# Kernel optimization log

Hardware: AMD Instinct MI355X
Metric: run time of the kernel (lower is better)

The kernel has to match this reference:

```python
import jax, jax.numpy as jnp
import numpy as np

EPS = 1e-5
HEADS, DK, DV = 8, 32, 64
SCALE = DK ** -0.5

def _bn(x, gamma, beta, mean, var):
    # eval-mode BatchNorm1d over channel dim of [b, c, n]
    inv = gamma / jnp.sqrt(var + EPS)
    return (x - mean[None, :, None]) * inv[None, :, None] + beta[None, :, None]

def setup_inputs() -> dict:
    key = jax.random.key(0)
    ks = jax.random.split(key, 24)
    dim, n, dim_out = 256, 1024, 256
    idk, idv = DK * HEADS, DV * HEADS
    def bn_params(k, c):
        k1, k2, k3, k4 = jax.random.split(k, 4)
        return (jax.random.normal(k1, (c,)) * 0.1 + 1.0,   # gamma
                jax.random.normal(k2, (c,)) * 0.1,          # beta
                jax.random.normal(k3, (c,)) * 0.1,          # running mean
                jax.random.uniform(k4, (c,)) * 0.5 + 0.5)   # running var > 0
    q_g, q_b, q_m, q_v = bn_params(ks[1], idk)
    k_g, k_b, k_m, k_v = bn_params(ks[2], idk)
    v_g, v_b, v_m, v_v = bn_params(ks[3], idv)
    o_g, o_b, o_m, o_v = bn_params(ks[4], dim_out)
    return {
        'x': jax.random.normal(ks[0], (8, dim, n), dtype=jnp.float32),
        'Wq': jax.random.normal(ks[5], (idk, dim)) * (dim ** -0.5),
        'Wk': jax.random.normal(ks[6], (idk, dim)) * (dim ** -0.5),
        'Wv': jax.random.normal(ks[7], (idv, dim)) * (dim ** -0.5),
        'Wo': jax.random.normal(ks[8], (dim_out, idv)) * (idv ** -0.5),
        'bo': jax.random.normal(ks[9], (dim_out,)) * 0.02,
        'pos_emb': jax.random.normal(ks[10], (n, HEADS)) * 0.02,
        'q_gamma': q_g, 'q_beta': q_b, 'q_mean': q_m, 'q_var': q_v,
        'k_gamma': k_g, 'k_beta': k_b, 'k_mean': k_m, 'k_var': k_v,
        'v_gamma': v_g, 'v_beta': v_b, 'v_mean': v_m, 'v_var': v_v,
        'o_gamma': o_g, 'o_beta': o_b, 'o_mean': o_m, 'o_var': o_v,
    }

def reference(x, Wq, Wk, Wv, Wo, bo, pos_emb,
              q_gamma, q_beta, q_mean, q_var,
              k_gamma, k_beta, k_mean, k_var,
              v_gamma, v_beta, v_mean, v_var,
              o_gamma, o_beta, o_mean, o_var):
    b, _, n = x.shape
    # 1x1 conv == channel matmul, then BN
    q = _bn(jnp.einsum('bcn,oc->bon', x, Wq), q_gamma, q_beta, q_mean, q_var)
    k = _bn(jnp.einsum('bcn,oc->bon', x, Wk), k_gamma, k_beta, k_mean, k_var)
    v = _bn(jnp.einsum('bcn,oc->bon', x, Wv), v_gamma, v_beta, v_mean, v_var)
    # b (h d) n -> b h n d
    q = q.reshape(b, HEADS, DK, n).transpose(0, 1, 3, 2)
    k = k.reshape(b, HEADS, DK, n).transpose(0, 1, 3, 2)
    v = v.reshape(b, HEADS, DV, n).transpose(0, 1, 3, 2)
    dots = jnp.einsum('bhid,bhjd->bhij', q, k) * SCALE
    # relative-position bias: emb[|i-j|] -> [n, n, h] -> [1, h, n, n]
    rel = jnp.abs(jnp.arange(n)[:, None] - jnp.arange(n)[None, :])
    bias = pos_emb[rel].transpose(2, 0, 1)[None]
    dots = dots + bias / SCALE
    attn = jax.nn.softmax(dots, axis=-1)
    out = jnp.einsum('bhij,bhjd->bhid', attn, v)
    # b h n d -> b (h d) n
    out = out.transpose(0, 1, 3, 2).reshape(b, HEADS * DV, n)
    out = jax.nn.gelu(out, approximate=False)
    out = jnp.einsum('bcn,oc->bon', out, Wo) + bo[None, :, None]
    return _bn(out, o_gamma, o_beta, o_mean, o_var)
```

## Files before the change

kernel.cpp:

```cpp
#include <hip/hip_runtime.h>
#include <hip/hip_bf16.h>

#define HEADS 8
#define DK 32
#define DV 64
#define DIM 256
#define NCTX 1024
#define NB 8
#define IDK 256
#define IDV 512
#define SCALE 0.17677669529663687f
#define INV_SCALE 5.656854249492381f
#define BN_EPS 1e-5f
#define THR 8.0f

typedef __bf16 bf16x8 __attribute__((ext_vector_type(8)));
typedef __bf16 bf16x4 __attribute__((ext_vector_type(4)));
typedef float f32x4 __attribute__((ext_vector_type(4)));
typedef float f32x16 __attribute__((ext_vector_type(16)));

static __device__ __forceinline__ unsigned short bfbits(float v) {
  __bf16 b = (__bf16)v;
  return __builtin_bit_cast(unsigned short, b);
}

__global__ __launch_bounds__(256) void k_prep_trans(
    const float* __restrict__ x,
    const float* __restrict__ Wq, const float* __restrict__ Wk,
    const float* __restrict__ Wv, const float* __restrict__ Wo,
    const float* __restrict__ bo, const float* __restrict__ pe,
    const float* __restrict__ qg, const float* __restrict__ qb,
    const float* __restrict__ qm, const float* __restrict__ qv,
    const float* __restrict__ kg, const float* __restrict__ kb,
    const float* __restrict__ km, const float* __restrict__ kv,
    const float* __restrict__ vg, const float* __restrict__ vb,
    const float* __restrict__ vm, const float* __restrict__ vv,
    const float* __restrict__ og, const float* __restrict__ ob,
    const float* __restrict__ om, const float* __restrict__ ov,
    __bf16* __restrict__ xT, __bf16* __restrict__ WB, float* __restrict__ BB,
    uint2* __restrict__ Tq4g) {
  int bid = blockIdx.x;
  if (bid < 1605) {
    int idx = bid * 256 + threadIdx.x;
    if (idx < 65536) {
      int o = idx >> 8;
      WB[idx] = (__bf16)(Wq[idx] * (qg[o] * rsqrtf(qv[o] + BN_EPS) * SCALE));
    } else if (idx < 131072) {
      int i = idx - 65536, o = i >> 8;
      WB[idx] = (__bf16)(Wk[i] * (kg[o] * rsqrtf(kv[o] + BN_EPS)));
    } else if (idx < 262144) {
      int i = idx - 131072, o = i >> 8;
      WB[idx] = (__bf16)(Wv[i] * (vg[o] * rsqrtf(vv[o] + BN_EPS)));
    } else if (idx < 393216) {
      int i = idx - 262144, o = i >> 9;
      WB[idx] = (__bf16)(Wo[i] * (og[o] * rsqrtf(ov[o] + BN_EPS)));
    } else if (idx < 394496) {
      int i = idx - 393216;
      if (i < 256) {
        float sc = qg[i] * rsqrtf(qv[i] + BN_EPS);
        BB[i] = (qb[i] - qm[i] * sc) * SCALE;
      } else if (i < 512) {
        int o = i - 256;
        float sc = kg[o] * rsqrtf(kv[o] + BN_EPS);
        BB[i] = kb[o] - km[o] * sc;
      } else if (i < 1024) {
        int o = i - 512;
        float sc = vg[o] * rsqrtf(vv[o] + BN_EPS);
        BB[i] = vb[o] - vm[o] * sc;
      } else {
        int o = i - 1024;
        float sc = og[o] * rsqrtf(ov[o] + BN_EPS);
        BB[i] = (bo[o] - om[o]) * sc + ob[o];
      }
    } else {
      int i = idx - 394496;
      int h = i >> 11, t = i & 2047;
      unsigned short us[4];
#pragma unroll
      for (int rr = 0; rr < 4; ++rr) {
        int d = t - rr - 1023; d = d < 0 ? -d : d; d = d > 1023 ? 1023 : d;
        us[rr] = bfbits(pe[(size_t)d * HEADS + h] * INV_SCALE);
      }
      uint2 e;
      e.x = (unsigned)us[0] | ((unsigned)us[1] << 16);
      e.y = (unsigned)us[2] | ((unsigned)us[3] << 16);
      Tq4g[((size_t)h << 11) + t] = e;
    }
  } else {
    __shared__ float t[64][65];
    int tb = bid - 1605;
    int b = tb >> 6, c0 = ((tb >> 4) & 3) * 64, n0 = (tb & 15) * 64;
    int col = threadIdx.x & 63, rb = threadIdx.x >> 6;
    const float* xp = x + ((size_t)b * DIM + c0) * NCTX + n0;
#pragma unroll
    for (int r = 0; r < 16; ++r) {
      int row = rb + 4 * r;
      t[row][col] = xp[(size_t)row * NCTX + col];
    }
    __syncthreads();
    __bf16* op = xT + ((size_t)b * NCTX + n0) * DIM + c0;
#pragma unroll
    for (int r = 0; r < 16; ++r) {
      int i = rb + 4 * r;
      op[(size_t)i * DIM + col] = (__bf16)t[col][i];
    }
  }
}

__global__ __launch_bounds__(256, 2) void k_gemm(
    const __bf16* __restrict__ Xsrc, const __bf16* __restrict__ Wsrc,
    const float* __restrict__ Bias, __bf16* __restrict__ Qws,
    __bf16* __restrict__ Kws, __bf16* __restrict__ Vws,
    float* __restrict__ Oout, int lda, int ksteps, int mode_base) {
  int bx = blockIdx.x, by = blockIdx.y;
  int mode = (mode_base == 3) ? 3 : (by < 2 ? 0 : (by < 4 ? 1 : 2));
  int tid = threadIdx.x, wave = tid >> 6, lane = tid & 63;
  int wm = wave >> 1, wn = wave & 1;
  int l16 = lane & 15, g = (lane >> 4) & 3, g4 = g * 4;
  int R0 = bx * 128;

  __shared__ __align__(16) char XTl[16384];
  __shared__ __align__(16) char WTl[16384];

  int sr = tid >> 1, sh = tid & 1;
  const __bf16* xg = Xsrc + (size_t)(R0 + sr) * lda + sh * 32;
  const __bf16* wg = Wsrc + (size_t)(by * 128 + sr) * lda + sh * 32;
  int wbase = sr * 128;
  int gsw[4];
#pragma unroll
  for (int q = 0; q < 4; ++q) gsw[q] = ((sh * 4 + q) ^ (sr & 7)) * 16;

  bf16x8 sx[4], sw[4];
#pragma unroll
  for (int q = 0; q < 4; ++q) {
    sx[q] = *reinterpret_cast<const bf16x8*>(xg + q * 8);
    sw[q] = *reinterpret_cast<const bf16x8*>(wg + q * 8);
  }

  f32x4 acc[4][4] = {};
  const char* Abase = (mode <= 1) ? WTl : XTl;
  const char* Bbase = (mode <= 1) ? XTl : WTl;

  for (int st = 0; st < ksteps; ++st) {
    __syncthreads();
#pragma unroll
    for (int q = 0; q < 4; ++q) {
      *reinterpret_cast<bf16x8*>(XTl + wbase + gsw[q]) = sx[q];
      *reinterpret_cast<bf16x8*>(WTl + wbase + gsw[q]) = sw[q];
    }
    __syncthreads();
    if (st + 1 < ksteps) {
      const __bf16* xn = xg + (st + 1) * 64;
      const __bf16* wn_ = wg + (st + 1) * 64;
#pragma unroll
      for (int q = 0; q < 4; ++q) {
        sx[q] = *reinterpret_cast<const bf16x8*>(xn + q * 8);
        sw[q] = *reinterpret_cast<const bf16x8*>(wn_ + q * 8);
      }
    }
#pragma unroll
    for (int kc = 0; kc < 2; ++kc) {
      bf16x8 af[4], bf[4];
#pragma unroll
      for (int t = 0; t < 4; ++t) {
        int ra = wm * 64 + t * 16 + l16;
        af[t] = *reinterpret_cast<const bf16x8*>(
            Abase + ra * 128 + (((kc * 4 + g) ^ (ra & 7)) * 16));
        int rb = wn * 64 + t * 16 + l16;
        bf[t] = *reinterpret_cast<const bf16x8*>(
            Bbase + rb * 128 + (((kc * 4 + g) ^ (rb & 7)) * 16));
      }
#pragma unroll
      for (int mt = 0; mt < 4; ++mt)
#pragma unroll
        for (int nt = 0; nt < 4; ++nt)
          acc[mt][nt] = __builtin_amdgcn_mfma_f32_16x16x32_bf16(
              af[mt], bf[nt], acc[mt][nt], 0, 0, 0);
    }
  }

  if (mode <= 1) {
    __bf16* OWS = (mode == 0) ? Qws : Kws;
    const float* bb = Bias + (mode == 0 ? 0 : 256);
    int oq0 = by * 128 - (mode == 1 ? 256 : 0) + wm * 64;
#pragma unroll
    for (int mt = 0; mt < 4; ++mt) {
      int oq = oq0 + mt * 16 + g4;
      float4 b4 = *reinterpret_cast<const float4*>(&bb[oq]);
      int h = oq >> 5, d0 = oq & 31;
#pragma unroll
      for (int nt = 0; nt < 4; ++nt) {
        int i = R0 + wn * 64 + nt * 16 + l16;
        int b = i >> 10, n = i & 1023;
        bf16x4 pk;
        pk[0] = (__bf16)(acc[mt][nt][0] + b4.x);
        pk[1] = (__bf16)(acc[mt][nt][1] + b4.y);
        pk[2] = (__bf16)(acc[mt][nt][2] + b4.z);
        pk[3] = (__bf16)(acc[mt][nt][3] + b4.w);
        *reinterpret_cast<bf16x4*>(
            &OWS[(((size_t)b * HEADS + h) * NCTX + n) * DK + d0]) = pk;
      }
    }
  } else if (mode == 2) {
#pragma unroll
    for (int nt = 0; nt < 4; ++nt) {
      int vo = (by - 4) * 128 + wn * 64 + nt * 16 + l16;
      float bia = Bias[512 + vo];
#pragma unroll
      for (int mt = 0; mt < 4; ++mt) {
        int i0 = R0 + wm * 64 + mt * 16 + g4;
        int b = i0 >> 10, n = i0 & 1023;
        bf16x4 pk;
#pragma unroll
        for (int rr = 0; rr < 4; ++rr) pk[rr] = (__bf16)(acc[mt][nt][rr] + bia);
        *reinterpret_cast<bf16x4*>(&Vws[((size_t)b * IDV + vo) * NCTX + n]) = pk;
      }
    }
  } else {
#pragma unroll
    for (int nt = 0; nt < 4; ++nt) {
      int o = by * 128 + wn * 64 + nt * 16 + l16;
      float bia = Bias[o];
#pragma unroll
      for (int mt = 0; mt < 4; ++mt) {
        int i0 = R0 + wm * 64 + mt * 16 + g4;
        int b = i0 >> 10, n = i0 & 1023;
        float4 st;
        st.x = acc[mt][nt][0] + bia;
        st.y = acc[mt][nt][1] + bia;
        st.z = acc[mt][nt][2] + bia;
        st.w = acc[mt][nt][3] + bia;
        *reinterpret_cast<float4*>(&Oout[((size_t)b * DIM + o) * NCTX + n]) = st;
      }
    }
  }
}

__global__ __launch_bounds__(256, 2) void k_attn(
    const __bf16* __restrict__ Qws, const __bf16* __restrict__ Kws,
    const __bf16* __restrict__ Vws, const uint2* __restrict__ Tq4g,
    __bf16* __restrict__ G) {
  int flat = blockIdx.x;
  int swz = (flat & 7) * 64 + (flat >> 3);
  int iblk = swz & 7, bh = swz >> 3;
  int b = bh >> 3, h = bh & 7;
  int tid = threadIdx.x, wave = tid >> 6, lane = tid & 63;
  int l31 = lane & 31, hi = lane >> 5;

  __shared__ __align__(16) __bf16 Klds[64][40];
  __shared__ __align__(16) __bf16 Vlds[64 * 64];
  __shared__ __align__(16) uint2 TqL[1152];

  int i0b = iblk * 128;
  {
    const uint4* tg4 = reinterpret_cast<const uint4*>(Tq4g + ((size_t)h << 11) + i0b);
    uint4* tl4 = reinterpret_cast<uint4*>(TqL);
    for (int c = tid; c < 576; c += 256) tl4[c] = tg4[c];
  }

  int i0w = i0b + wave * 32;
  int irow = i0w + l31;
  const __bf16* qbase = Qws + (size_t)bh * NCTX * DK;
  const __bf16* kbase = Kws + (size_t)bh * NCTX * DK;
  const __bf16* vbase = Vws + ((size_t)b * IDV + h * DV) * NCTX;
  bf16x8 qf0 = *reinterpret_cast<const bf16x8*>(qbase + (size_t)irow * DK + 8 * hi);
  bf16x8 qf1 = *reinterpret_cast<const bf16x8*>(qbase + (size_t)irow * DK + 16 + 8 * hi);

  int r_ = tid >> 2, sk = tid & 3;
  const __bf16* kgp = kbase + (size_t)r_ * DK + 8 * sk;
  const __bf16* vgp = vbase + (size_t)r_ * NCTX + 8 * sk;
  __bf16* kw = &Klds[r_][8 * sk];
  __bf16* vw0 = Vlds + r_ * 64 + 8 * (sk ^ (r_ & 7));
  __bf16* vw1 = Vlds + r_ * 64 + 8 * ((sk + 4) ^ (r_ & 7));

  bf16x8 rk = *reinterpret_cast<const bf16x8*>(kgp);
  bf16x8 rv0 = *reinterpret_cast<const bf16x8*>(vgp);
  bf16x8 rv1 = *reinterpret_cast<const bf16x8*>(vgp + 32);

  f32x16 acc0 = {}, acc1 = {};
  float m = -1e30f, s = 0.0f;
  int kxb = wave * 32 + l31 + 1023 - 4 * hi;
  const bf16x4* Tqp = reinterpret_cast<const bf16x4*>(TqL);

  for (int it = 0; it < 16; ++it) {
    int j0 = it * 64;
    __syncthreads();
    *reinterpret_cast<bf16x8*>(kw) = rk;
    *reinterpret_cast<bf16x8*>(vw0) = rv0;
    *reinterpret_cast<bf16x8*>(vw1) = rv1;
    __syncthreads();
    int jn = (j0 + 64) & (NCTX - 1);
    rk = *reinterpret_cast<const bf16x8*>(kgp + (size_t)jn * DK);
    rv0 = *reinterpret_cast<const bf16x8*>(vgp + jn);
    rv1 = *reinterpret_cast<const bf16x8*>(vgp + jn + 32);

    float sv[32];
#pragma unroll
    for (int jg = 0; jg < 2; ++jg) {
      bf16x8 kf0 = *reinterpret_cast<const bf16x8*>(&Klds[32 * jg + l31][8 * hi]);
      bf16x8 kf1 = *reinterpret_cast<const bf16x8*>(&Klds[32 * jg + l31][16 + 8 * hi]);
      f32x16 S = {};
      S = __builtin_amdgcn_mfma_f32_32x32x16_bf16(kf0, qf0, S, 0, 0, 0);
      S = __builtin_amdgcn_mfma_f32_32x32x16_bf16(kf1, qf1, S, 0, 0, 0);
      int kb_ = kxb - j0 - 32 * jg;
#pragma unroll
      for (int q = 0; q < 4; ++q) {
        bf16x4 q4 = Tqp[kb_ - 8 * q];
#pragma unroll
        for (int rr = 0; rr < 4; ++rr)
          sv[jg * 16 + q * 4 + rr] = S[q * 4 + rr] + (float)q4[rr];
      }
    }
    float pmax = sv[0];
#pragma unroll
    for (int k = 1; k < 32; ++k) pmax = fmaxf(pmax, sv[k]);
    if (__any(pmax > m + THR)) {
      float mx = fmaxf(pmax, __shfl_xor(pmax, 32));
      float mnew = fmaxf(m, mx);
      float corr = __expf(m - mnew);
      s *= corr; m = mnew;
#pragma unroll
      for (int r = 0; r < 16; ++r) {
        float cv = __shfl(corr, (r & 3) + 8 * (r >> 2) + 4 * hi);
        acc0[r] *= cv; acc1[r] *= cv;
      }
    }
#pragma unroll
    for (int k = 0; k < 32; ++k) sv[k] = __expf(sv[k] - m);
    float ps = 0.0f;
#pragma unroll
    for (int k = 0; k < 32; ++k) ps += sv[k];
    s += ps;
#pragma unroll
    for (int jg = 0; jg < 2; ++jg) {
#pragma unroll
      for (int u = 0; u < 2; ++u) {
        int base = jg * 16 + 8 * u;
        unsigned we0, we1, wo0, wo1;
        asm("v_cvt_pk_bf16_f32 %0, %1, %2" : "=v"(we0) : "v"(sv[base + 0]), "v"(sv[base + 1]));
        asm("v_cvt_pk_bf16_f32 %0, %1, %2" : "=v"(we1) : "v"(sv[base + 2]), "v"(sv[base + 3]));
        asm("v_cvt_pk_bf16_f32 %0, %1, %2" : "=v"(wo0) : "v"(sv[base + 4]), "v"(sv[base + 5]));
        asm("v_cvt_pk_bf16_f32 %0, %1, %2" : "=v"(wo1) : "v"(sv[base + 6]), "v"(sv[base + 7]));
        asm volatile("v_permlane32_swap_b32 %0, %1" : "+v"(we0), "+v"(wo0));
        asm volatile("v_permlane32_swap_b32 %0, %1" : "+v"(we1), "+v"(wo1));
        uint4 pw = {we0, we1, wo0, wo1};
        bf16x8 pfrag = *reinterpret_cast<bf16x8*>(&pw);
        int c = jg * 2 + u;
        int sl = 2 * c + hi;
        bf16x8 vf0 = *reinterpret_cast<const bf16x8*>(Vlds + l31 * 64 + 8 * (sl ^ (l31 & 7)));
        bf16x8 vf1 = *reinterpret_cast<const bf16x8*>(Vlds + (32 + l31) * 64 + 8 * (sl ^ (l31 & 7)));
        acc0 = __builtin_amdgcn_mfma_f32_32x32x16_bf16(pfrag, vf0, acc0, 0, 0, 0);
        acc1 = __builtin_amdgcn_mfma_f32_32x32x16_bf16(pfrag, vf1, acc1, 0, 0, 0);
      }
    }
  }
  float srow = s + __shfl_xor(s, 32);
  float inv = 1.0f / srow;
  __bf16* gbase = G + (size_t)b * NCTX * IDV + h * DV + l31;
#pragma unroll
  for (int r = 0; r < 16; ++r) {
    int il = (r & 3) + 8 * (r >> 2) + 4 * hi;
    float iv = __shfl(inv, il);
    float v0 = acc0[r] * iv, v1 = acc1[r] * iv;
    float g0 = 0.5f * v0 * (1.0f + erff(v0 * 0.70710678118654752f));
    float g1 = 0.5f * v1 * (1.0f + erff(v1 * 0.70710678118654752f));
    gbase[(size_t)(i0w + il) * IDV] = (__bf16)g0;
    gbase[(size_t)(i0w + il) * IDV + 32] = (__bf16)g1;
  }
}

extern "C" void kernel_launch(void* const* d_in, const int* in_sizes, int n_in,
                              void* d_out, int out_size, void* d_ws, size_t ws_size,
                              hipStream_t stream) {
  const float* x  = (const float*)d_in[0];
  const float* Wq = (const float*)d_in[1];
  const float* Wk = (const float*)d_in[2];
  const float* Wv = (const float*)d_in[3];
  const float* Wo = (const float*)d_in[4];
  const float* bo = (const float*)d_in[5];
  const float* pe = (const float*)d_in[6];
  const float* qg = (const float*)d_in[7];
  const float* qb = (const float*)d_in[8];
  const float* qm = (const float*)d_in[9];
  const float* qv = (const float*)d_in[10];
  const float* kg = (const float*)d_in[11];
  const float* kb = (const float*)d_in[12];
  const float* km = (const float*)d_in[13];
  const float* kv = (const float*)d_in[14];
  const float* vg = (const float*)d_in[15];
  const float* vb = (const float*)d_in[16];
  const float* vm = (const float*)d_in[17];
  const float* vv = (const float*)d_in[18];
  const float* og = (const float*)d_in[19];
  const float* ob = (const float*)d_in[20];
  const float* om = (const float*)d_in[21];
  const float* ov = (const float*)d_in[22];

  char* ws = (char*)d_ws;
  __bf16* xT = (__bf16*)(ws);
  __bf16* Q  = (__bf16*)(ws + (4ull << 20));
  __bf16* K  = (__bf16*)(ws + (8ull << 20));
  __bf16* V  = (__bf16*)(ws + (12ull << 20));
  __bf16* G  = (__bf16*)(ws + (20ull << 20));
  __bf16* WB = (__bf16*)(ws + (28ull << 20));
  float*  BB = (float*)(ws + (28ull << 20) + (768ull << 10));
  uint2*  Tq = (uint2*)(ws + (29ull << 20));
  float* out = (float*)d_out;

  k_prep_trans<<<dim3(2117), 256, 0, stream>>>(
      x, Wq, Wk, Wv, Wo, bo, pe, qg, qb, qm, qv, kg, kb, km, kv,
      vg, vb, vm, vv, og, ob, om, ov, xT, WB, BB, Tq);
  k_gemm<<<dim3(64, 8), 256, 0, stream>>>(xT, WB, BB, Q, K, V, nullptr,
                                          DIM, 4, 0);
  k_attn<<<dim3(512), 256, 0, stream>>>(Q, K, V, Tq, G);
  k_gemm<<<dim3(64, 2), 256, 0, stream>>>(G, WB + 262144, BB + 1024,
                                          nullptr, nullptr, nullptr, out,
                                          IDV, 8, 3);
}
```

Before: 63.57 us.

## Use exp2 softmax, smaller attention blocks, split output GEMM, MFMA priority hints

Measured after the change: 60.64 us. 4.6% less time.

```diff
diff --git a/kernel.cpp b/kernel.cpp
--- a/kernel.cpp
+++ b/kernel.cpp
@@ -11,8 +11,9 @@
 #define IDV 512
 #define SCALE 0.17677669529663687f
 #define INV_SCALE 5.656854249492381f
+#define LOG2E 1.4426950408889634f
 #define BN_EPS 1e-5f
-#define THR 8.0f
+#define THR 11.5416f
 
 typedef __bf16 bf16x8 __attribute__((ext_vector_type(8)));
 typedef __bf16 bf16x4 __attribute__((ext_vector_type(4)));
@@ -44,7 +45,7 @@
     int idx = bid * 256 + threadIdx.x;
     if (idx < 65536) {
       int o = idx >> 8;
-      WB[idx] = (__bf16)(Wq[idx] * (qg[o] * rsqrtf(qv[o] + BN_EPS) * SCALE));
+      WB[idx] = (__bf16)(Wq[idx] * (qg[o] * rsqrtf(qv[o] + BN_EPS) * SCALE * LOG2E));
     } else if (idx < 131072) {
       int i = idx - 65536, o = i >> 8;
       WB[idx] = (__bf16)(Wk[i] * (kg[o] * rsqrtf(kv[o] + BN_EPS)));
@@ -58,7 +59,7 @@
       int i = idx - 393216;
       if (i < 256) {
         float sc = qg[i] * rsqrtf(qv[i] + BN_EPS);
-        BB[i] = (qb[i] - qm[i] * sc) * SCALE;
+        BB[i] = (qb[i] - qm[i] * sc) * SCALE * LOG2E;
       } else if (i < 512) {
         int o = i - 256;
         float sc = kg[o] * rsqrtf(kv[o] + BN_EPS);
@@ -79,7 +80,7 @@
 #pragma unroll
       for (int rr = 0; rr < 4; ++rr) {
         int d = t - rr - 1023; d = d < 0 ? -d : d; d = d > 1023 ? 1023 : d;
-        us[rr] = bfbits(pe[(size_t)d * HEADS + h] * INV_SCALE);
+        us[rr] = bfbits(pe[(size_t)d * HEADS + h] * INV_SCALE * LOG2E);
       }
       uint2 e;
       e.x = (unsigned)us[0] | ((unsigned)us[1] << 16);
@@ -107,13 +108,12 @@
   }
 }
 
-__global__ __launch_bounds__(256, 2) void k_gemm(
+__global__ __launch_bounds__(256, 2) void k_gemm_qkv(
     const __bf16* __restrict__ Xsrc, const __bf16* __restrict__ Wsrc,
     const float* __restrict__ Bias, __bf16* __restrict__ Qws,
-    __bf16* __restrict__ Kws, __bf16* __restrict__ Vws,
-    float* __restrict__ Oout, int lda, int ksteps, int mode_base) {
+    __bf16* __restrict__ Kws, __bf16* __restrict__ Vws) {
   int bx = blockIdx.x, by = blockIdx.y;
-  int mode = (mode_base == 3) ? 3 : (by < 2 ? 0 : (by < 4 ? 1 : 2));
+  int mode = by < 2 ? 0 : (by < 4 ? 1 : 2);
   int tid = threadIdx.x, wave = tid >> 6, lane = tid & 63;
   int wm = wave >> 1, wn = wave & 1;
   int l16 = lane & 15, g = (lane >> 4) & 3, g4 = g * 4;
@@ -123,8 +123,8 @@
   __shared__ __align__(16) char WTl[16384];
 
   int sr = tid >> 1, sh = tid & 1;
-  const __bf16* xg = Xsrc + (size_t)(R0 + sr) * lda + sh * 32;
-  const __bf16* wg = Wsrc + (size_t)(by * 128 + sr) * lda + sh * 32;
+  const __bf16* xg = Xsrc + (size_t)(R0 + sr) * DIM + sh * 32;
+  const __bf16* wg = Wsrc + (size_t)(by * 128 + sr) * DIM + sh * 32;
   int wbase = sr * 128;
   int gsw[4];
 #pragma unroll
@@ -141,7 +141,7 @@
   const char* Abase = (mode <= 1) ? WTl : XTl;
   const char* Bbase = (mode <= 1) ? XTl : WTl;
 
-  for (int st = 0; st < ksteps; ++st) {
+  for (int st = 0; st < 4; ++st) {
     __syncthreads();
 #pragma unroll
     for (int q = 0; q < 4; ++q) {
@@ -149,7 +149,7 @@
       *reinterpret_cast<bf16x8*>(WTl + wbase + gsw[q]) = sw[q];
     }
     __syncthreads();
-    if (st + 1 < ksteps) {
+    if (st + 1 < 4) {
       const __bf16* xn = xg + (st + 1) * 64;
       const __bf16* wn_ = wg + (st + 1) * 64;
 #pragma unroll
@@ -170,12 +170,14 @@
         bf[t] = *reinterpret_cast<const bf16x8*>(
             Bbase + rb * 128 + (((kc * 4 + g) ^ (rb & 7)) * 16));
       }
+      __builtin_amdgcn_s_setprio(1);
 #pragma unroll
       for (int mt = 0; mt < 4; ++mt)
 #pragma unroll
         for (int nt = 0; nt < 4; ++nt)
           acc[mt][nt] = __builtin_amdgcn_mfma_f32_16x16x32_bf16(
               af[mt], bf[nt], acc[mt][nt], 0, 0, 0);
+      __builtin_amdgcn_s_setprio(0);
     }
   }
 
@@ -201,7 +203,7 @@
             &OWS[(((size_t)b * HEADS + h) * NCTX + n) * DK + d0]) = pk;
       }
     }
-  } else if (mode == 2) {
+  } else {
 #pragma unroll
     for (int nt = 0; nt < 4; ++nt) {
       int vo = (by - 4) * 128 + wn * 64 + nt * 16 + l16;
@@ -216,46 +218,121 @@
         *reinterpret_cast<bf16x4*>(&Vws[((size_t)b * IDV + vo) * NCTX + n]) = pk;
       }
     }
-  } else {
-#pragma unroll
-    for (int nt = 0; nt < 4; ++nt) {
-      int o = by * 128 + wn * 64 + nt * 16 + l16;
-      float bia = Bias[o];
-#pragma unroll
-      for (int mt = 0; mt < 4; ++mt) {
-        int i0 = R0 + wm * 64 + mt * 16 + g4;
-        int b = i0 >> 10, n = i0 & 1023;
-        float4 st;
-        st.x = acc[mt][nt][0] + bia;
-        st.y = acc[mt][nt][1] + bia;
-        st.z = acc[mt][nt][2] + bia;
-        st.w = acc[mt][nt][3] + bia;
-        *reinterpret_cast<float4*>(&Oout[((size_t)b * DIM + o) * NCTX + n]) = st;
-      }
-    }
   }
 }
 
-__global__ __launch_bounds__(256, 2) void k_attn(
+__global__ __launch_bounds__(256, 2) void k_gemm_out(
+    const __bf16* __restrict__ G, const __bf16* __restrict__ WoB,
+    const float* __restrict__ bo2, float* __restrict__ out) {
+  int bx = blockIdx.x, by = blockIdx.y;
+  int tid = threadIdx.x, wave = tid >> 6, lane = tid & 63;
+  int wm = wave >> 1, wn = wave & 1;
+  int l16 = lane & 15, g = (lane >> 4) & 3, g4 = g * 4;
+  int R0 = bx * 128;
+
+  __shared__ __align__(16) char XTl[16384];
+  __shared__ __align__(16) char WTl[8192];
+
+  int sr = tid >> 1, sh = tid & 1;
+  const __bf16* xg = G + (size_t)(R0 + sr) * IDV + sh * 32;
+  int xbase = sr * 128;
+  int gsw[4];
+#pragma unroll
+  for (int q = 0; q < 4; ++q) gsw[q] = ((sh * 4 + q) ^ (sr & 7)) * 16;
+
+  int wsr = tid >> 2, wq = tid & 3;
+  const __bf16* wg = WoB + (size_t)(by * 64 + wsr) * IDV + wq * 16;
+  int wbase = wsr * 128;
+  int gswW[2];
+#pragma unroll
+  for (int q = 0; q < 2; ++q) gswW[q] = ((wq * 2 + q) ^ (wsr & 7)) * 16;
+
+  bf16x8 sx[4], sw[2];
+#pragma unroll
+  for (int q = 0; q < 4; ++q) sx[q] = *reinterpret_cast<const bf16x8*>(xg + q * 8);
+#pragma unroll
+  for (int q = 0; q < 2; ++q) sw[q] = *reinterpret_cast<const bf16x8*>(wg + q * 8);
+
+  f32x4 acc[4][2] = {};
+
+  for (int st = 0; st < 8; ++st) {
+    __syncthreads();
+#pragma unroll
+    for (int q = 0; q < 4; ++q) *reinterpret_cast<bf16x8*>(XTl + xbase + gsw[q]) = sx[q];
+#pragma unroll
+    for (int q = 0; q < 2; ++q) *reinterpret_cast<bf16x8*>(WTl + wbase + gswW[q]) = sw[q];
+    __syncthreads();
+    if (st + 1 < 8) {
+      const __bf16* xn = xg + (st + 1) * 64;
+      const __bf16* wn_ = wg + (st + 1) * 64;
+#pragma unroll
+      for (int q = 0; q < 4; ++q) sx[q] = *reinterpret_cast<const bf16x8*>(xn + q * 8);
+#pragma unroll
+      for (int q = 0; q < 2; ++q) sw[q] = *reinterpret_cast<const bf16x8*>(wn_ + q * 8);
+    }
+#pragma unroll
+    for (int kc = 0; kc < 2; ++kc) {
+      bf16x8 af[4], bf[2];
+#pragma unroll
+      for (int t = 0; t < 4; ++t) {
+        int ra = wm * 64 + t * 16 + l16;
+        af[t] = *reinterpret_cast<const bf16x8*>(
+            XTl + ra * 128 + (((kc * 4 + g) ^ (ra & 7)) * 16));
+      }
+#pragma unroll
+      for (int t = 0; t < 2; ++t) {
+        int rb = wn * 32 + t * 16 + l16;
+        bf[t] = *reinterpret_cast<const bf16x8*>(
+            WTl + rb * 128 + (((kc * 4 + g) ^ (rb & 7)) * 16));
+      }
+      __builtin_amdgcn_s_setprio(1);
+#pragma unroll
+      for (int mt = 0; mt < 4; ++mt)
+#pragma unroll
+        for (int nt = 0; nt < 2; ++nt)
+          acc[mt][nt] = __builtin_amdgcn_mfma_f32_16x16x32_bf16(
+              af[mt], bf[nt], acc[mt][nt], 0, 0, 0);
+      __builtin_amdgcn_s_setprio(0);
+    }
+  }
+#pragma unroll
+  for (int nt = 0; nt < 2; ++nt) {
+    int o = by * 64 + wn * 32 + nt * 16 + l16;
+    float bia = bo2[o];
+#pragma unroll
+    for (int mt = 0; mt < 4; ++mt) {
+      int i0 = R0 + wm * 64 + mt * 16 + g4;
+      int b = i0 >> 10, n = i0 & 1023;
+      float4 st;
+      st.x = acc[mt][nt][0] + bia;
+      st.y = acc[mt][nt][1] + bia;
+      st.z = acc[mt][nt][2] + bia;
+      st.w = acc[mt][nt][3] + bia;
+      *reinterpret_cast<float4*>(&out[((size_t)b * DIM + o) * NCTX + n]) = st;
+    }
+  }
+}
+
+__global__ __launch_bounds__(128, 3) void k_attn(
     const __bf16* __restrict__ Qws, const __bf16* __restrict__ Kws,
     const __bf16* __restrict__ Vws, const uint2* __restrict__ Tq4g,
     __bf16* __restrict__ G) {
   int flat = blockIdx.x;
-  int swz = (flat & 7) * 64 + (flat >> 3);
-  int iblk = swz & 7, bh = swz >> 3;
+  int swz = (flat & 7) * 128 + (flat >> 3);
+  int iblk = swz & 15, bh = swz >> 4;
   int b = bh >> 3, h = bh & 7;
   int tid = threadIdx.x, wave = tid >> 6, lane = tid & 63;
   int l31 = lane & 31, hi = lane >> 5;
 
   __shared__ __align__(16) __bf16 Klds[64][40];
   __shared__ __align__(16) __bf16 Vlds[64 * 64];
-  __shared__ __align__(16) uint2 TqL[1152];
-
-  int i0b = iblk * 128;
+  __shared__ __align__(16) uint2 TqL[1088];
+
+  int i0b = iblk * 64;
   {
     const uint4* tg4 = reinterpret_cast<const uint4*>(Tq4g + ((size_t)h << 11) + i0b);
     uint4* tl4 = reinterpret_cast<uint4*>(TqL);
-    for (int c = tid; c < 576; c += 256) tl4[c] = tg4[c];
+    for (int c = tid; c < 544; c += 128) tl4[c] = tg4[c];
   }
 
   int i0w = i0b + wave * 32;
@@ -266,16 +343,22 @@
   bf16x8 qf0 = *reinterpret_cast<const bf16x8*>(qbase + (size_t)irow * DK + 8 * hi);
   bf16x8 qf1 = *reinterpret_cast<const bf16x8*>(qbase + (size_t)irow * DK + 16 + 8 * hi);
 
-  int r_ = tid >> 2, sk = tid & 3;
-  const __bf16* kgp = kbase + (size_t)r_ * DK + 8 * sk;
-  const __bf16* vgp = vbase + (size_t)r_ * NCTX + 8 * sk;
-  __bf16* kw = &Klds[r_][8 * sk];
-  __bf16* vw0 = Vlds + r_ * 64 + 8 * (sk ^ (r_ & 7));
-  __bf16* vw1 = Vlds + r_ * 64 + 8 * ((sk + 4) ^ (r_ & 7));
-
-  bf16x8 rk = *reinterpret_cast<const bf16x8*>(kgp);
+  int r_ = tid >> 1, s2 = (tid & 1) * 2;
+  const __bf16* kgp = kbase + (size_t)r_ * DK + 8 * s2;
+  const __bf16* vgp = vbase + (size_t)r_ * NCTX + 8 * s2;
+  __bf16* kw0 = &Klds[r_][8 * s2];
+  __bf16* kw1 = &Klds[r_][8 * (s2 + 1)];
+  __bf16* vw0 = Vlds + r_ * 64 + 8 * ((s2) ^ (r_ & 7));
+  __bf16* vw1 = Vlds + r_ * 64 + 8 * ((s2 + 1) ^ (r_ & 7));
+  __bf16* vw2 = Vlds + r_ * 64 + 8 * ((s2 + 4) ^ (r_ & 7));
+  __bf16* vw3 = Vlds + r_ * 64 + 8 * ((s2 + 5) ^ (r_ & 7));
+
+  bf16x8 rk0 = *reinterpret_cast<const bf16x8*>(kgp);
+  bf16x8 rk1 = *reinterpret_cast<const bf16x8*>(kgp + 8);
   bf16x8 rv0 = *reinterpret_cast<const bf16x8*>(vgp);
-  bf16x8 rv1 = *reinterpret_cast<const bf16x8*>(vgp + 32);
+  bf16x8 rv1 = *reinterpret_cast<const bf16x8*>(vgp + 8);
+  bf16x8 rv2 = *reinterpret_cast<const bf16x8*>(vgp + 32);
+  bf16x8 rv3 = *reinterpret_cast<const bf16x8*>(vgp + 40);
 
   f32x16 acc0 = {}, acc1 = {};
   float m = -1e30f, s = 0.0f;
@@ -285,14 +368,20 @@
   for (int it = 0; it < 16; ++it) {
     int j0 = it * 64;
     __syncthreads();
-    *reinterpret_cast<bf16x8*>(kw) = rk;
+    *reinterpret_cast<bf16x8*>(kw0) = rk0;
+    *reinterpret_cast<bf16x8*>(kw1) = rk1;
     *reinterpret_cast<bf16x8*>(vw0) = rv0;
     *reinterpret_cast<bf16x8*>(vw1) = rv1;
+    *reinterpret_cast<bf16x8*>(vw2) = rv2;
+    *reinterpret_cast<bf16x8*>(vw3) = rv3;
     __syncthreads();
     int jn = (j0 + 64) & (NCTX - 1);
-    rk = *reinterpret_cast<const bf16x8*>(kgp + (size_t)jn * DK);
+    rk0 = *reinterpret_cast<const bf16x8*>(kgp + (size_t)jn * DK);
+    rk1 = *reinterpret_cast<const bf16x8*>(kgp + (size_t)jn * DK + 8);
     rv0 = *reinterpret_cast<const bf16x8*>(vgp + jn);
-    rv1 = *reinterpret_cast<const bf16x8*>(vgp + jn + 32);
+    rv1 = *reinterpret_cast<const bf16x8*>(vgp + jn + 8);
+    rv2 = *reinterpret_cast<const bf16x8*>(vgp + jn + 32);
+    rv3 = *reinterpret_cast<const bf16x8*>(vgp + jn + 40);
 
     float sv[32];
 #pragma unroll
@@ -300,8 +389,10 @@
       bf16x8 kf0 = *reinterpret_cast<const bf16x8*>(&Klds[32 * jg + l31][8 * hi]);
       bf16x8 kf1 = *reinterpret_cast<const bf16x8*>(&Klds[32 * jg + l31][16 + 8 * hi]);
       f32x16 S = {};
+      __builtin_amdgcn_s_setprio(1);
       S = __builtin_amdgcn_mfma_f32_32x32x16_bf16(kf0, qf0, S, 0, 0, 0);
       S = __builtin_amdgcn_mfma_f32_32x32x16_bf16(kf1, qf1, S, 0, 0, 0);
+      __builtin_amdgcn_s_setprio(0);
       int kb_ = kxb - j0 - 32 * jg;
 #pragma unroll
       for (int q = 0; q < 4; ++q) {
@@ -317,7 +408,7 @@
     if (__any(pmax > m + THR)) {
       float mx = fmaxf(pmax, __shfl_xor(pmax, 32));
       float mnew = fmaxf(m, mx);
-      float corr = __expf(m - mnew);
+      float corr = __builtin_amdgcn_exp2f(m - mnew);
       s *= corr; m = mnew;
 #pragma unroll
       for (int r = 0; r < 16; ++r) {
@@ -326,7 +417,7 @@
       }
     }
 #pragma unroll
-    for (int k = 0; k < 32; ++k) sv[k] = __expf(sv[k] - m);
+    for (int k = 0; k < 32; ++k) sv[k] = __builtin_amdgcn_exp2f(sv[k] - m);
     float ps = 0.0f;
 #pragma unroll
     for (int k = 0; k < 32; ++k) ps += sv[k];
@@ -349,8 +440,10 @@
         int sl = 2 * c + hi;
         bf16x8 vf0 = *reinterpret_cast<const bf16x8*>(Vlds + l31 * 64 + 8 * (sl ^ (l31 & 7)));
         bf16x8 vf1 = *reinterpret_cast<const bf16x8*>(Vlds + (32 + l31) * 64 + 8 * (sl ^ (l31 & 7)));
+        __builtin_amdgcn_s_setprio(1);
         acc0 = __builtin_amdgcn_mfma_f32_32x32x16_bf16(pfrag, vf0, acc0, 0, 0, 0);
         acc1 = __builtin_amdgcn_mfma_f32_32x32x16_bf16(pfrag, vf1, acc1, 0, 0, 0);
+        __builtin_amdgcn_s_setprio(0);
       }
     }
   }
@@ -410,10 +503,7 @@
   k_prep_trans<<<dim3(2117), 256, 0, stream>>>(
       x, Wq, Wk, Wv, Wo, bo, pe, qg, qb, qm, qv, kg, kb, km, kv,
       vg, vb, vm, vv, og, ob, om, ov, xT, WB, BB, Tq);
-  k_gemm<<<dim3(64, 8), 256, 0, stream>>>(xT, WB, BB, Q, K, V, nullptr,
-                                          DIM, 4, 0);
-  k_attn<<<dim3(512), 256, 0, stream>>>(Q, K, V, Tq, G);
-  k_gemm<<<dim3(64, 2), 256, 0, stream>>>(G, WB + 262144, BB + 1024,
-                                          nullptr, nullptr, nullptr, out,
-                                          IDV, 8, 3);
+  k_gemm_qkv<<<dim3(64, 8), 256, 0, stream>>>(xT, WB, BB, Q, K, V);
+  k_attn<<<dim3(1024), 128, 0, stream>>>(Q, K, V, Tq, G);
+  k_gemm_out<<<dim3(64, 4), 256, 0, stream>>>(G, WB + 262144, BB + 1024, out);
 }
```
